# Kernel tuning notes

Hardware: AMD Instinct MI355X
Metric: run time of the kernel (lower is better)

The kernel has to match this reference:

```python
import jax, jax.numpy as jnp
from jax import lax
import numpy as np

S = 4          # tile_length
T = 16         # tile_size = S**2
K = 7          # length_inter_tile
NI = 49        # num_inter = K**2
CH_DE = 7      # design channels
EPS = 0.01
NEG = 0.01     # LeakyReLU default slope


def _conv(x, w, b, stride, pad):
    y = lax.conv_general_dilated(x, w, (stride, stride), [(pad, pad), (pad, pad)],
                                 dimension_numbers=('NCHW', 'OIHW', 'NCHW'))
    return y + b[None, :, None, None]


def _lrelu(x):
    return jax.nn.leaky_relu(x, NEG)


def _unfold(x, k=K):
    # torch F.unfold(x, k, padding=k//2): (B,C,H,W) -> (B, C*k*k, H*W), (c,i,j) ordering
    pad = k // 2
    B, C, H, W = x.shape
    xp = jnp.pad(x, ((0, 0), (0, 0), (pad, pad), (pad, pad)))
    cols = jnp.stack([xp[:, :, i:i + H, j:j + W] for i in range(k) for j in range(k)], axis=2)
    return cols.reshape(B, C * k * k, H * W)


def setup_inputs():
    key = jax.random.key(0)
    ks = jax.random.split(key, 16)
    B, H, W = 1, 48, 48
    CIN = 10; CF = 100; CW = 1024
    FINAL = T * T * NI  # 12544
    HALF = FINAL // 2   # 6272
    def w_init(k, shape, fan_in):
        return jax.random.normal(k, shape, jnp.float32) * np.float32(np.sqrt(2.0 / fan_in))
    return {
        'input': jax.random.normal(ks[0], (B, T, CIN, H, W), jnp.float32),
        'design': jax.random.normal(ks[1], (B, T, CH_DE, H, W), jnp.float32),
        'fw0': w_init(ks[2], (CF, CIN, 3, 3), CIN * 9),
        'fb0': jnp.zeros((CF,), jnp.float32),
        'fw_rest': w_init(ks[3], (13, CF, CF, 3, 3), CF * 9),
        'fb_rest': jnp.zeros((13, CF), jnp.float32),
        'ww0': w_init(ks[4], (CW, CF, S, S), CF * S * S),
        'wb0': jnp.zeros((CW,), jnp.float32),
        'ww_mid': w_init(ks[5], (3, CW, CW, 3, 3), CW * 9),
        'wb_mid': jnp.zeros((3, CW), jnp.float32),
        'ww1': w_init(ks[6], (HALF, CW, 1, 1), CW),
        'wb1': jnp.zeros((HALF,), jnp.float32),
        'ww2': w_init(ks[7], (FINAL, HALF, 1, 1), HALF),
        'wb2': jnp.zeros((FINAL,), jnp.float32),
    }


def reference(input, design, fw0, fb0, fw_rest, fb_rest, ww0, wb0, ww_mid, wb_mid, ww1, wb1, ww2, wb2):
    B, _, CIN, H, W = input.shape
    hw = H * W
    # domain: (B*hw, T, CH_DE)
    domain = design.transpose(0, 3, 4, 1, 2).reshape(B * hw, T, CH_DE)
    # X from unfolded design: (B*hw*NI, T, CH_DE)
    u = _unfold(design.reshape(B, T * CH_DE, H, W))
    X = u.reshape(B, T * CH_DE, NI, hw).transpose(0, 3, 2, 1).reshape(B * hw * NI, T, CH_DE)
    # make_full_res_img: stack tile (s*i + j) -> spatial offset (i, j)
    full = input.reshape(B, S, S, CIN, H, W).transpose(0, 3, 4, 1, 5, 2).reshape(B, CIN, H * S, W * S)
    # feature network: 14 conv3x3 + LeakyReLU at full res
    f = _lrelu(_conv(full, fw0, fb0, 1, 1))
    for i in range(fw_rest.shape[0]):
        f = _lrelu(_conv(f, fw_rest[i], fb_rest[i], 1, 1))
    g = _lrelu(_conv(f, ww0, wb0, S, 0))
    for i in range(ww_mid.shape[0]):
        g = _lrelu(_conv(g, ww_mid[i], wb_mid[i], 1, 1))
    g = _lrelu(_conv(g, ww1, wb1, 1, 0))
    Wmap = jnp.tanh(_conv(g, ww2, wb2, 1, 0))  # (B, NI*T*T, H, W)
    Wm = Wmap.reshape(B, NI, T, T, H, W).transpose(0, 4, 5, 1, 2, 3).reshape(B * hw * NI, T, T)
    Wm = Wm @ Wm.transpose(0, 2, 1) + jnp.eye(T, dtype=Wm.dtype)
    # normal equations
    XTW = X.transpose(0, 2, 1) @ Wm                                  # (N, CH_DE, T)
    A = (XTW @ X).reshape(B * hw, NI, CH_DE, CH_DE).sum(axis=1)
    A = A + EPS * jnp.eye(CH_DE, dtype=A.dtype)
    # all 3 color channels at once (same math as per-channel loop)
    Yu = _unfold(input[:, :, :3].reshape(B, T * 3, H, W))            # (B, T*3*NI, hw)
    Y = Yu.reshape(B, T, 3, NI, hw).transpose(0, 4, 3, 1, 2).reshape(B * hw * NI, T, 3)
    Bv = (XTW @ Y).reshape(B * hw, NI, CH_DE, 3).sum(axis=1)         # (B*hw, CH_DE, 3)
    para = jnp.linalg.solve(A, Bv)                                   # (B*hw, CH_DE, 3)
    out = (domain @ para).reshape(B, H, W, T, 3).transpose(0, 3, 4, 1, 2)
    return out
```

## Files before the change

kernel.cpp:

```cpp
#include <hip/hip_runtime.h>
#include <math.h>

#define LRELU(v) ((v) > 0.f ? (v) : 0.01f * (v))

typedef __attribute__((ext_vector_type(8))) short bf8v;
typedef __attribute__((ext_vector_type(4))) float f4v;

static __device__ __forceinline__ unsigned short f2b(float f) {
    unsigned int u = __float_as_uint(f);
    unsigned int r = (u + 0x7fffu + ((u >> 16) & 1u)) >> 16;
    return (unsigned short)r;
}

static __device__ __forceinline__ void gload16(const unsigned short* g, unsigned short* l) {
    __builtin_amdgcn_global_load_lds(
        (__attribute__((address_space(1))) void*)(g),
        (__attribute__((address_space(3))) void*)(l), 16, 0, 0);
}

__global__ __launch_bounds__(256) void k_build_full(const float* __restrict__ in,
                                                    unsigned short* __restrict__ full0p) {
    int idx = blockIdx.x * 256 + threadIdx.x;
    if (idx >= 368640) return;
    int c = idx % 10, pix = idx / 10;
    int X = pix % 192, Y = pix / 192;
    int t = (Y & 3) * 4 + (X & 3);
    int h = Y >> 2, w = X >> 2;
    int pp = (Y + 1) * 194 + (X + 1);
    full0p[(size_t)pp * 16 + c] = f2b(in[(((t * 10 + c) * 48) + h) * 48 + w]);
}

template <int C, int CP, int Q>
__global__ __launch_bounds__(256) void k_wcvt(const float* __restrict__ src,
                                              unsigned short* __restrict__ dst,
                                              int Mv, int Kp) {
    int m = blockIdx.x;
    for (int kp = threadIdx.x; kp < Kp; kp += 256) {
        int qq = kp / CP, c = kp - qq * CP;
        float v = 0.f;
        if (m < Mv && c < C && qq < Q)
            v = src[((size_t)m * C + c) * Q + qq];
        dst[(size_t)m * Kp + kp] = f2b(v);
    }
}

__global__ __launch_bounds__(256) void k_cvt_flat(const float* __restrict__ src,
                                                  unsigned short* __restrict__ dst,
                                                  size_t n) {
    size_t i = ((size_t)blockIdx.x * 256 + threadIdx.x) * 4;
    if (i >= n) return;
    float4 v = *(const float4*)(src + i);
    ushort4 o;
    o.x = f2b(v.x); o.y = f2b(v.y); o.z = f2b(v.z); o.w = f2b(v.w);
    *(ushort4*)(dst + i) = o;
}

__global__ __launch_bounds__(256) void k_im2col4(const unsigned short* __restrict__ src,
                                                 unsigned short* __restrict__ dst) {
    int p = blockIdx.x;
    int x = p % 48, y = p / 48;
    for (int kp = threadIdx.x; kp < 1600; kp += 256) {
        int qq = kp / 100, c = kp - qq * 100;
        int yy = y * 4 + (qq >> 2), xx = x * 4 + (qq & 3);
        dst[(size_t)p * 1600 + kp] = src[(size_t)((yy + 1) * 194 + (xx + 1)) * 104 + c];
    }
}

template <int ACT, int OF32, int REMAP, int SWZ>
__global__ __launch_bounds__(256) void k_gemm(
    const unsigned short* __restrict__ A, const unsigned short* __restrict__ Bt,
    const float* __restrict__ bias, void* __restrict__ outv,
    int K, int Mv, int ldout) {
    __shared__ __align__(16) unsigned short As[128 * 32];
    __shared__ __align__(16) unsigned short Bs[128 * 32];
    const int tid = threadIdx.x;
    const int lane = tid & 63;
    const int w = tid >> 6;
    const int wm = w >> 1, wn = w & 1;
    const int q = lane >> 4, ln = lane & 15;
    int bx = blockIdx.x, by = blockIdx.y;
    if (SWZ) {
        int gx = gridDim.x;
        int nwg = gx * gridDim.y;
        int lin = by * gx + bx;
        int qq = nwg >> 3, rr = nwg & 7;
        int xcd = lin & 7, idx = lin >> 3;
        int wg = (xcd < rr ? xcd * (qq + 1) : rr * (qq + 1) + (xcd - rr) * qq) + idx;
        bx = wg % gx; by = wg / gx;
    }
    const int m0 = by * 128, n0 = bx * 128;

    f4v acc[4][4];
#pragma unroll
    for (int i = 0; i < 4; ++i)
#pragma unroll
        for (int j = 0; j < 4; ++j) acc[i][j] = (f4v){0.f, 0.f, 0.f, 0.f};

    const int br0 = tid >> 2, bk0 = (tid & 3) << 3;
    const unsigned short* pA0 = A + (size_t)(m0 + br0) * K + bk0;
    const unsigned short* pA1 = pA0 + (size_t)64 * K;
    const unsigned short* pB0 = Bt + (size_t)(n0 + br0) * K + bk0;
    const unsigned short* pB1 = pB0 + (size_t)64 * K;
    unsigned short* lA0 = As + tid * 8;
    unsigned short* lA1 = As + 2048 + tid * 8;
    unsigned short* lB0 = Bs + tid * 8;
    unsigned short* lB1 = Bs + 2048 + tid * 8;
    const unsigned short* Ap2 = &As[(wm * 64 + ln) * 32 + q * 8];
    const unsigned short* Bp2 = &Bs[(wn * 64 + ln) * 32 + q * 8];

    for (int k0 = 0; k0 < K; k0 += 32) {
        gload16(pA0 + k0, lA0);
        gload16(pA1 + k0, lA1);
        gload16(pB0 + k0, lB0);
        gload16(pB1 + k0, lB1);
        __syncthreads();
        bf8v af[4], bfv[4];
#pragma unroll
        for (int i = 0; i < 4; ++i) af[i] = *(const bf8v*)(Ap2 + i * 512);
#pragma unroll
        for (int j = 0; j < 4; ++j) bfv[j] = *(const bf8v*)(Bp2 + j * 512);
#pragma unroll
        for (int i = 0; i < 4; ++i)
#pragma unroll
            for (int j = 0; j < 4; ++j)
                acc[i][j] = __builtin_amdgcn_mfma_f32_16x16x32_bf16(af[i], bfv[j], acc[i][j], 0, 0, 0);
        __syncthreads();
    }

    float* tb = ((float*)As) + w * 288;
#pragma unroll
    for (int i = 0; i < 4; ++i) {
        const int mbase = m0 + wm * 64 + i * 16;
        float bi[4];
#pragma unroll
        for (int r = 0; r < 4; ++r) {
            int mm = mbase + q * 4 + r;
            bi[r] = (mm < Mv) ? bias[mm] : 0.f;
        }
#pragma unroll
        for (int j = 0; j < 4; ++j) {
            const int nbase = n0 + wn * 64 + j * 16;
#pragma unroll
            for (int r = 0; r < 4; ++r) {
                float v = acc[i][j][r] + bi[r];
                v = ACT ? tanhf(v) : LRELU(v);
                tb[ln * 17 + q * 4 + r] = v;
            }
#pragma unroll
            for (int r = 0; r < 4; ++r) {
                float v = tb[(q * 4 + r) * 17 + ln];
                int n = nbase + q * 4 + r;
                int m = mbase + ln;
                if (m < Mv) {
                    if (REMAP == 3) {
                        int y = n / 48, x = n - y * 48;
                        size_t np = (size_t)((y + 1) * 50 + x + 1);
                        ((unsigned short*)outv)[np * (size_t)ldout + m] = f2b(v);
                    } else {
                        if (OF32) ((float*)outv)[(size_t)n * ldout + m] = v;
                        else ((unsigned short*)outv)[(size_t)n * ldout + m] = f2b(v);
                    }
                }
            }
        }
    }
}

template <int ACT, int OF32, int SWZ>
__global__ __launch_bounds__(512, 1) void k_gemm256(
    const unsigned short* __restrict__ A, const unsigned short* __restrict__ Bt,
    const float* __restrict__ bias, void* __restrict__ outv,
    int K, int Mv, int ldout) {
    __shared__ __align__(16) unsigned short As[2][16384];
    __shared__ __align__(16) unsigned short Bs[2][16384];
    const int tid = threadIdx.x;
    const int lane = tid & 63;
    const int w = tid >> 6;
    const int wm = w >> 2;
    const int wn = w & 3;
    const int q = lane >> 4, ln = lane & 15;

    int bx = blockIdx.x, by = blockIdx.y;
    if (SWZ) {
        int gx = gridDim.x;
        int nwg = gx * gridDim.y;
        int lin = by * gx + bx;
        int qq = nwg >> 3, rr = nwg & 7;
        int xcd = lin & 7, idx = lin >> 3;
        int wg = (xcd < rr ? xcd * (qq + 1) : rr * (qq + 1) + (xcd - rr) * qq) + idx;
        bx = wg % gx; by = wg / gx;
    }
    const int m0 = by * 256, n0 = bx * 256;

    f4v acc[8][4];
#pragma unroll
    for (int i = 0; i < 8; ++i)
#pragma unroll
        for (int j = 0; j < 4; ++j) acc[i][j] = (f4v){0.f, 0.f, 0.f, 0.f};

    const int srow = tid >> 3;
    const int sj = tid & 7;
    const int sjx = sj ^ (srow & 7);
    const unsigned short* gA = A + (size_t)(m0 + srow) * K + sjx * 8;
    const unsigned short* gB = Bt + (size_t)(n0 + srow) * K + sjx * 8;
    const size_t rstride = (size_t)64 * K;
    unsigned short* lA = &As[0][0] + tid * 8;
    unsigned short* lB = &Bs[0][0] + tid * 8;

#define STAGE256(buf, t)                                               \
    {                                                                  \
        const unsigned short* ga_ = gA + (size_t)(t) * 64;             \
        const unsigned short* gb_ = gB + (size_t)(t) * 64;             \
        unsigned short* la_ = lA + (buf) * 16384;                      \
        unsigned short* lb_ = lB + (buf) * 16384;                      \
        _Pragma("unroll")                                              \
        for (int r_ = 0; r_ < 4; ++r_) {                               \
            gload16(ga_ + r_ * rstride, la_ + r_ * 4096);              \
            gload16(gb_ + r_ * rstride, lb_ + r_ * 4096);              \
        }                                                              \
    }

    int aoff[8], boff[4];
#pragma unroll
    for (int mf = 0; mf < 8; ++mf) aoff[mf] = (wm * 128 + mf * 16 + ln) * 64;
#pragma unroll
    for (int nf = 0; nf < 4; ++nf) boff[nf] = (wn * 64 + nf * 16 + ln) * 64;
    const int l7 = ln & 7;
    const int koff0 = ((0 * 4 + q) ^ l7) * 8;
    const int koff1 = ((1 * 4 + q) ^ l7) * 8;

    const int NT = K >> 6;
    STAGE256(0, 0);
    STAGE256(1, 1);
    asm volatile("s_waitcnt vmcnt(8)" ::: "memory");
    __builtin_amdgcn_sched_barrier(0);
    __builtin_amdgcn_s_barrier();

    bf8v a0[8], b0[4], a1[8], b1[4];

    {
        const unsigned short* as = &As[0][0];
        const unsigned short* bs = &Bs[0][0];
#pragma unroll
        for (int mf = 0; mf < 8; ++mf) a0[mf] = *(const bf8v*)&as[aoff[mf] + koff0];
#pragma unroll
        for (int nf = 0; nf < 4; ++nf) b0[nf] = *(const bf8v*)&bs[boff[nf] + koff0];
#pragma unroll
        for (int mf = 0; mf < 8; ++mf) a1[mf] = *(const bf8v*)&as[aoff[mf] + koff1];
#pragma unroll
        for (int nf = 0; nf < 4; ++nf) b1[nf] = *(const bf8v*)&bs[boff[nf] + koff1];
        __builtin_amdgcn_s_setprio(1);
#pragma unroll
        for (int mf = 0; mf < 8; ++mf)
#pragma unroll
            for (int nf = 0; nf < 4; ++nf)
                acc[mf][nf] = __builtin_amdgcn_mfma_f32_16x16x32_bf16(a0[mf], b0[nf], acc[mf][nf], 0, 0, 0);
        __builtin_amdgcn_s_setprio(0);
        asm volatile("s_waitcnt lgkmcnt(0)" ::: "memory");
        __builtin_amdgcn_sched_barrier(0);
        __builtin_amdgcn_s_barrier();
        if (2 < NT) {
            STAGE256(0, 2);
            asm volatile("s_waitcnt vmcnt(8)" ::: "memory");
        } else {
            asm volatile("s_waitcnt vmcnt(0)" ::: "memory");
        }
        __builtin_amdgcn_sched_barrier(0);
        __builtin_amdgcn_s_barrier();
    }

    for (int t = 1; t < NT; ++t) {
        const int cur = t & 1;
        const unsigned short* as = &As[cur][0];
        const unsigned short* bs = &Bs[cur][0];
#pragma unroll
        for (int mf = 0; mf < 8; ++mf) a0[mf] = *(const bf8v*)&as[aoff[mf] + koff0];
#pragma unroll
        for (int nf = 0; nf < 4; ++nf) b0[nf] = *(const bf8v*)&bs[boff[nf] + koff0];
        __builtin_amdgcn_s_setprio(1);
#pragma unroll
        for (int mf = 0; mf < 8; ++mf)
#pragma unroll
            for (int nf = 0; nf < 4; ++nf)
                acc[mf][nf] = __builtin_amdgcn_mfma_f32_16x16x32_bf16(a1[mf], b1[nf], acc[mf][nf], 0, 0, 0);
        __builtin_amdgcn_s_setprio(0);
#pragma unroll
        for (int mf = 0; mf < 8; ++mf) a1[mf] = *(const bf8v*)&as[aoff[mf] + koff1];
#pragma unroll
        for (int nf = 0; nf < 4; ++nf) b1[nf] = *(const bf8v*)&bs[boff[nf] + koff1];
        __builtin_amdgcn_s_setprio(1);
#pragma unroll
        for (int mf = 0; mf < 8; ++mf)
#pragma unroll
            for (int nf = 0; nf < 4; ++nf)
                acc[mf][nf] = __builtin_amdgcn_mfma_f32_16x16x32_bf16(a0[mf], b0[nf], acc[mf][nf], 0, 0, 0);
        __builtin_amdgcn_s_setprio(0);
        asm volatile("s_waitcnt lgkmcnt(0)" ::: "memory");
        __builtin_amdgcn_sched_barrier(0);
        __builtin_amdgcn_s_barrier();
        if (t + 2 < NT) {
            STAGE256(cur, t + 2);
            asm volatile("s_waitcnt vmcnt(8)" ::: "memory");
        } else {
            asm volatile("s_waitcnt vmcnt(0)" ::: "memory");
        }
        __builtin_amdgcn_sched_barrier(0);
        __builtin_amdgcn_s_barrier();
    }
    __builtin_amdgcn_s_setprio(1);
#pragma unroll
    for (int mf = 0; mf < 8; ++mf)
#pragma unroll
        for (int nf = 0; nf < 4; ++nf)
            acc[mf][nf] = __builtin_amdgcn_mfma_f32_16x16x32_bf16(a1[mf], b1[nf], acc[mf][nf], 0, 0, 0);
    __builtin_amdgcn_s_setprio(0);
    __builtin_amdgcn_s_barrier();
#undef STAGE256

    float* tb = ((float*)&As[0][0]) + w * 288;
#pragma unroll
    for (int mf = 0; mf < 8; ++mf) {
        const int mbase = m0 + wm * 128 + mf * 16;
        float bi[4];
#pragma unroll
        for (int r = 0; r < 4; ++r) {
            int mm = mbase + q * 4 + r;
            bi[r] = (mm < Mv) ? bias[mm] : 0.f;
        }
#pragma unroll
        for (int nf = 0; nf < 4; ++nf) {
            const int nbase = n0 + wn * 64 + nf * 16;
#pragma unroll
            for (int r = 0; r < 4; ++r) {
                float v = acc[mf][nf][r] + bi[r];
                v = ACT ? tanhf(v) : LRELU(v);
                tb[ln * 17 + q * 4 + r] = v;
            }
#pragma unroll
            for (int r = 0; r < 4; ++r) {
                float v = tb[(q * 4 + r) * 17 + ln];
                int n = nbase + q * 4 + r;
                int m = mbase + ln;
                if (m < Mv) {
                    if (OF32) ((float*)outv)[(size_t)n * ldout + m] = v;
                    else ((unsigned short*)outv)[(size_t)n * ldout + m] = f2b(v);
                }
            }
        }
    }
}

template <int TAPK, int CST, int SH, int REMAP>
__global__ __launch_bounds__(256) void k_cgemm(
    const unsigned short* __restrict__ A, const unsigned short* __restrict__ Bt,
    const float* __restrict__ bias, unsigned short* __restrict__ outp,
    int Mv, int ldout) {
    __shared__ __align__(16) unsigned short As[128 * 32];
    __shared__ __align__(16) unsigned short Bs[128 * 32];
    const int tid = threadIdx.x;
    const int lane = tid & 63;
    const int w = tid >> 6;
    const int wm = w >> 1, wn = w & 1;
    const int q = lane >> 4, ln = lane & 15;
    const int m0 = blockIdx.y * 128, n0 = blockIdx.x * 128;
    const int KA = 9 * TAPK;

    f4v acc[4][4];
#pragma unroll
    for (int i = 0; i < 4; ++i)
#pragma unroll
        for (int j = 0; j < 4; ++j) acc[i][j] = (f4v){0.f, 0.f, 0.f, 0.f};

    const int br0 = tid >> 2, bk0 = (tid & 3) << 3;
    const unsigned short* pA0 = A + (size_t)(m0 + br0) * KA + bk0;
    const unsigned short* pA1 = pA0 + (size_t)64 * KA;
    unsigned short* lA0 = As + tid * 8;
    unsigned short* lA1 = As + 2048 + tid * 8;
    unsigned short* lB0 = Bs + tid * 8;
    unsigned short* lB1 = Bs + 2048 + tid * 8;
    const unsigned short* Ap2 = &As[(wm * 64 + ln) * 32 + q * 8];
    const unsigned short* Bp2 = &Bs[(wn * 64 + ln) * 32 + q * 8];

#pragma unroll
    for (int tap = 0; tap < 9; ++tap) {
        const int sh = (tap / 3 - 1) * SH + (tap % 3 - 1);
        const unsigned short* pB0 = Bt + (long)(n0 + br0 + sh) * CST + bk0;
        const unsigned short* pB1 = pB0 + (long)64 * CST;
        const int kab = tap * TAPK;
        for (int kk = 0; kk < TAPK; kk += 32) {
            gload16(pA0 + kab + kk, lA0);
            gload16(pA1 + kab + kk, lA1);
            gload16(pB0 + kk, lB0);
            gload16(pB1 + kk, lB1);
            __syncthreads();
            bf8v af[4], bfv[4];
#pragma unroll
            for (int i = 0; i < 4; ++i) af[i] = *(const bf8v*)(Ap2 + i * 512);
#pragma unroll
            for (int j = 0; j < 4; ++j) bfv[j] = *(const bf8v*)(Bp2 + j * 512);
#pragma unroll
            for (int i = 0; i < 4; ++i)
#pragma unroll
                for (int j = 0; j < 4; ++j)
                    acc[i][j] = __builtin_amdgcn_mfma_f32_16x16x32_bf16(af[i], bfv[j], acc[i][j], 0, 0, 0);
            __syncthreads();
        }
    }

    float* tb = ((float*)As) + w * 288;
#pragma unroll
    for (int i = 0; i < 4; ++i) {
        const int mbase = m0 + wm * 64 + i * 16;
        float bi[4];
#pragma unroll
        for (int r = 0; r < 4; ++r) {
            int mm = mbase + q * 4 + r;
            bi[r] = (mm < Mv) ? bias[mm] : 0.f;
        }
#pragma unroll
        for (int j = 0; j < 4; ++j) {
            const int nbase = n0 + wn * 64 + j * 16;
#pragma unroll
            for (int r = 0; r < 4; ++r) {
                float v = acc[i][j][r] + bi[r];
                v = LRELU(v);
                tb[ln * 17 + q * 4 + r] = v;
            }
#pragma unroll
            for (int r = 0; r < 4; ++r) {
                float v = tb[(q * 4 + r) * 17 + ln];
                int n = nbase + q * 4 + r;
                int m = mbase + ln;
                if (m < Mv) {
                    if (REMAP == 1) {
                        int y = n / 194, x = n - y * 194;
                        bool z = (n >= 37636) || y == 0 || y >= 193 || x == 0 || x >= 193;
                        outp[(size_t)n * ldout + m] = f2b(z ? 0.f : v);
                    } else if (REMAP == 2) {
                        int y = n / 50, x = n - y * 50;
                        bool z = (n >= 2500) || y == 0 || y >= 49 || x == 0 || x >= 49;
                        outp[(size_t)n * ldout + m] = f2b(z ? 0.f : v);
                    } else if (REMAP == 4) {
                        int y = n / 50, x = n - y * 50;
                        if (n < 2500 && y >= 1 && y <= 48 && x >= 1 && x <= 48)
                            outp[(size_t)((y - 1) * 48 + (x - 1)) * ldout + m] = f2b(v);
                    }
                }
            }
        }
    }
}

template <int TAPK, int CST, int SH, int REMAP>
__global__ __launch_bounds__(256) void k_cgemm64(
    const unsigned short* __restrict__ A, const unsigned short* __restrict__ Bt,
    const float* __restrict__ bias, unsigned short* __restrict__ outp,
    int Mv, int ldout) {
    __shared__ __align__(16) unsigned short As[64 * 32];
    __shared__ __align__(16) unsigned short Bs[128 * 32];
    const int tid = threadIdx.x;
    const int lane = tid & 63;
    const int wn = tid >> 6;
    const int q = lane >> 4, ln = lane & 15;
    const int m0 = blockIdx.y * 64, n0 = blockIdx.x * 128;
    const int KA = 9 * TAPK;

    f4v acc[4][2];
#pragma unroll
    for (int i = 0; i < 4; ++i)
#pragma unroll
        for (int j = 0; j < 2; ++j) acc[i][j] = (f4v){0.f, 0.f, 0.f, 0.f};

    const int br0 = tid >> 2, bk0 = (tid & 3) << 3;
    const unsigned short* pA0 = A + (size_t)(m0 + br0) * KA + bk0;
    unsigned short* lA0 = As + tid * 8;
    unsigned short* lB0 = Bs + tid * 8;
    unsigned short* lB1 = Bs + 2048 + tid * 8;
    const unsigned short* Ap2 = &As[ln * 32 + q * 8];
    const unsigned short* Bp2 = &Bs[(wn * 32 + ln) * 32 + q * 8];

#pragma unroll
    for (int tap = 0; tap < 9; ++tap) {
        const int sh = (tap / 3 - 1) * SH + (tap % 3 - 1);
        const unsigned short* pB0 = Bt + (long)(n0 + br0 + sh) * CST + bk0;
        const unsigned short* pB1 = pB0 + (long)64 * CST;
        const int kab = tap * TAPK;
        for (int kk = 0; kk < TAPK; kk += 32) {
            gload16(pA0 + kab + kk, lA0);
            gload16(pB0 + kk, lB0);
            gload16(pB1 + kk, lB1);
            __syncthreads();
            bf8v af[4], bfv[2];
#pragma unroll
            for (int i = 0; i < 4; ++i) af[i] = *(const bf8v*)(Ap2 + i * 512);
#pragma unroll
            for (int j = 0; j < 2; ++j) bfv[j] = *(const bf8v*)(Bp2 + j * 512);
#pragma unroll
            for (int i = 0; i < 4; ++i)
#pragma unroll
                for (int j = 0; j < 2; ++j)
                    acc[i][j] = __builtin_amdgcn_mfma_f32_16x16x32_bf16(af[i], bfv[j], acc[i][j], 0, 0, 0);
            __syncthreads();
        }
    }

    float* tb = ((float*)Bs) + wn * 288;
#pragma unroll
    for (int i = 0; i < 4; ++i) {
        const int mbase = m0 + i * 16;
        float bi[4];
#pragma unroll
        for (int r = 0; r < 4; ++r) {
            int mm = mbase + q * 4 + r;
            bi[r] = (mm < Mv) ? bias[mm] : 0.f;
        }
#pragma unroll
        for (int j = 0; j < 2; ++j) {
            const int nbase = n0 + wn * 32 + j * 16;
#pragma unroll
            for (int r = 0; r < 4; ++r) {
                float v = acc[i][j][r] + bi[r];
                v = LRELU(v);
                tb[ln * 17 + q * 4 + r] = v;
            }
#pragma unroll
            for (int r = 0; r < 4; ++r) {
                float v = tb[(q * 4 + r) * 17 + ln];
                int n = nbase + q * 4 + r;
                int m = mbase + ln;
                if (m < Mv) {
                    if (REMAP == 2) {
                        int y = n / 50, x = n - y * 50;
                        bool z = (n >= 2500) || y == 0 || y >= 49 || x == 0 || x >= 49;
                        outp[(size_t)n * ldout + m] = f2b(z ? 0.f : v);
                    } else if (REMAP == 4) {
                        int y = n / 50, x = n - y * 50;
                        if (n < 2500 && y >= 1 && y <= 48 && x >= 1 && x <= 48)
                            outp[(size_t)((y - 1) * 48 + (x - 1)) * ldout + m] = f2b(v);
                    }
                }
            }
        }
    }
}

template <int ACT, int OF32, int AF32>
__global__ __launch_bounds__(256) void k_gemm_f32a(
    const void* __restrict__ Ain, const unsigned short* __restrict__ Bt,
    const float* __restrict__ bias, void* __restrict__ outv,
    int K, int Mv, int ldout) {
    __shared__ __align__(16) unsigned short As[128 * 40];
    __shared__ __align__(16) unsigned short Bs[128 * 40];
    const int tid = threadIdx.x;
    const int lane = tid & 63;
    const int w = tid >> 6;
    const int wm = w >> 1, wn = w & 1;
    const int q = lane >> 4, ln = lane & 15;
    const int m0 = blockIdx.y * 128, n0 = blockIdx.x * 128;

    f4v acc[4][4];
#pragma unroll
    for (int i = 0; i < 4; ++i)
#pragma unroll
        for (int j = 0; j < 4; ++j) acc[i][j] = (f4v){0.f, 0.f, 0.f, 0.f};

    const int br0 = tid >> 2, bk0 = (tid & 3) << 3;
    const int br1 = br0 + 64;
    const int bl0 = br0 * 40 + bk0, bl1 = br1 * 40 + bk0;
    const unsigned short* pB0 = Bt + (size_t)(n0 + br0) * K + bk0;
    const unsigned short* pB1 = Bt + (size_t)(n0 + br1) * K + bk0;

    const unsigned short* Ab = (const unsigned short*)Ain;
    const float* Af = (const float*)Ain;
    const unsigned short* pA0 = Ab + (size_t)(m0 + br0) * K + bk0;
    const unsigned short* pA1 = Ab + (size_t)(m0 + br1) * K + bk0;
    const int fr = tid >> 3, fk = (tid & 7) << 2;
    const float* pF = Af + (size_t)(m0 + fr) * K + fk;

    for (int k0 = 0; k0 < K; k0 += 32) {
        if (AF32) {
#pragma unroll
            for (int jj = 0; jj < 4; ++jj) {
                float4 v = *(const float4*)(pF + (size_t)jj * 32 * K + k0);
                unsigned int lo = ((unsigned)f2b(v.y) << 16) | f2b(v.x);
                unsigned int hi = ((unsigned)f2b(v.w) << 16) | f2b(v.z);
                *(uint2*)&As[(fr + jj * 32) * 40 + fk] = make_uint2(lo, hi);
            }
        } else {
            uint4 a0 = *(const uint4*)(pA0 + k0);
            uint4 a1 = *(const uint4*)(pA1 + k0);
            *(uint4*)&As[bl0] = a0;
            *(uint4*)&As[bl1] = a1;
        }
        uint4 b0 = *(const uint4*)(pB0 + k0);
        uint4 b1 = *(const uint4*)(pB1 + k0);
        *(uint4*)&Bs[bl0] = b0;
        *(uint4*)&Bs[bl1] = b1;
        __syncthreads();
        const unsigned short* Ap2 = &As[(wm * 64 + ln) * 40 + q * 8];
        const unsigned short* Bp2 = &Bs[(wn * 64 + ln) * 40 + q * 8];
        bf8v af[4], bfv[4];
#pragma unroll
        for (int i = 0; i < 4; ++i) af[i] = *(const bf8v*)(Ap2 + i * 640);
#pragma unroll
        for (int j = 0; j < 4; ++j) bfv[j] = *(const bf8v*)(Bp2 + j * 640);
#pragma unroll
        for (int i = 0; i < 4; ++i)
#pragma unroll
            for (int j = 0; j < 4; ++j)
                acc[i][j] = __builtin_amdgcn_mfma_f32_16x16x32_bf16(af[i], bfv[j], acc[i][j], 0, 0, 0);
        __syncthreads();
    }

    float* tb = ((float*)As) + w * 288;
#pragma unroll
    for (int i = 0; i < 4; ++i) {
        const int mbase = m0 + wm * 64 + i * 16;
        float bi[4];
#pragma unroll
        for (int r = 0; r < 4; ++r) {
            int mm = mbase + q * 4 + r;
            bi[r] = (mm < Mv) ? bias[mm] : 0.f;
        }
#pragma unroll
        for (int j = 0; j < 4; ++j) {
            const int nbase = n0 + wn * 64 + j * 16;
#pragma unroll
            for (int r = 0; r < 4; ++r) {
                float v = acc[i][j][r] + bi[r];
                v = ACT ? tanhf(v) : LRELU(v);
                tb[ln * 17 + q * 4 + r] = v;
            }
#pragma unroll
            for (int r = 0; r < 4; ++r) {
                float v = tb[(q * 4 + r) * 17 + ln];
                size_t n = nbase + q * 4 + r;
                int m = mbase + ln;
                if (m < Mv) {
                    if (OF32) ((float*)outv)[n * (size_t)ldout + m] = v;
                    else ((unsigned short*)outv)[n * (size_t)ldout + m] = f2b(v);
                }
            }
        }
    }
}

__global__ __launch_bounds__(256) void k_solve(const float* __restrict__ WmT,
                                               const float* __restrict__ design,
                                               const float* __restrict__ input,
                                               float* __restrict__ out) {
    const int p = blockIdx.x;
    const int h = p / 48, wpx = p % 48;
    const int tid = threadIdx.x;
    __shared__ float Msh[16 * 17];
    __shared__ float Gsh[16 * 17];
    __shared__ float Xsh[16 * 8];
    __shared__ float Ysh[16 * 4];
    __shared__ float XTWsh[7 * 17];
    __shared__ float Aacc[49];
    __shared__ float Bacc[21];
    __shared__ float parash[21];

    if (tid < 49) Aacc[tid] = 0.f;
    if (tid >= 64 && tid < 85) Bacc[tid - 64] = 0.f;
    __syncthreads();

    const float* wrow = WmT + (size_t)p * 12544;
    for (int ni = 0; ni < 49; ++ni) {
        {
            int t1 = tid >> 4, t2 = tid & 15;
            Msh[t1 * 17 + t2] = wrow[ni * 256 + tid];
        }
        int sy = h + ni / 7 - 3, sx = wpx + ni % 7 - 3;
        bool inb = (sy >= 0 && sy < 48 && sx >= 0 && sx < 48);
        if (tid < 112) {
            int t = tid / 7, c = tid - t * 7;
            Xsh[t * 8 + c] = inb ? design[(size_t)(t * 7 + c) * 2304 + sy * 48 + sx] : 0.f;
        } else if (tid >= 128 && tid < 176) {
            int l = tid - 128;
            int t = l / 3, r = l - t * 3;
            Ysh[t * 4 + r] = inb ? input[(size_t)(t * 10 + r) * 2304 + sy * 48 + sx] : 0.f;
        }
        __syncthreads();
        {
            int t1 = tid >> 4, t2 = tid & 15;
            float s = (t1 == t2) ? 1.f : 0.f;
#pragma unroll
            for (int k = 0; k < 16; ++k) s += Msh[t1 * 17 + k] * Msh[t2 * 17 + k];
            Gsh[t1 * 17 + t2] = s;
        }
        __syncthreads();
        if (tid < 112) {
            int c = tid >> 4, t2 = tid & 15;
            float s = 0.f;
#pragma unroll
            for (int t1 = 0; t1 < 16; ++t1) s += Xsh[t1 * 8 + c] * Gsh[t1 * 17 + t2];
            XTWsh[c * 17 + t2] = s;
        }
        __syncthreads();
        if (tid < 49) {
            int c1 = tid / 7, c2 = tid - c1 * 7;
            float s = 0.f;
#pragma unroll
            for (int t = 0; t < 16; ++t) s += XTWsh[c1 * 17 + t] * Xsh[t * 8 + c2];
            Aacc[tid] += s;
        } else if (tid >= 64 && tid < 85) {
            int l = tid - 64;
            int c = l / 3, r = l - c * 3;
            float s = 0.f;
#pragma unroll
            for (int t = 0; t < 16; ++t) s += XTWsh[c * 17 + t] * Ysh[t * 4 + r];
            Bacc[l] += s;
        }
        __syncthreads();
    }

    if (tid == 0) {
        float Mg[7][10];
#pragma unroll
        for (int i = 0; i < 7; ++i) {
#pragma unroll
            for (int j = 0; j < 7; ++j) Mg[i][j] = Aacc[i * 7 + j] + ((i == j) ? 0.01f : 0.f);
#pragma unroll
            for (int r = 0; r < 3; ++r) Mg[i][7 + r] = Bacc[i * 3 + r];
        }
#pragma unroll
        for (int kk = 0; kk < 7; ++kk) {
            float inv = 1.f / Mg[kk][kk];
#pragma unroll
            for (int j = 0; j < 10; ++j) Mg[kk][j] *= inv;
#pragma unroll
            for (int i = 0; i < 7; ++i) {
                if (i == kk) continue;
                float f = Mg[i][kk];
#pragma unroll
                for (int j = 0; j < 10; ++j) Mg[i][j] -= f * Mg[kk][j];
            }
        }
#pragma unroll
        for (int c = 0; c < 7; ++c)
#pragma unroll
            for (int r = 0; r < 3; ++r) parash[c * 3 + r] = Mg[c][7 + r];
    }
    __syncthreads();

    if (tid < 48) {
        int t = tid / 3, r = tid - t * 3;
        float s = 0.f;
#pragma unroll
        for (int c = 0; c < 7; ++c)
            s += design[(size_t)(t * 7 + c) * 2304 + p] * parash[c * 3 + r];
        out[(size_t)tid * 2304 + p] = s;
    }
}

extern "C" void kernel_launch(void* const* d_in, const int* in_sizes, int n_in,
                              void* d_out, int out_size, void* d_ws, size_t ws_size,
                              hipStream_t stream) {
    const float* input   = (const float*)d_in[0];
    const float* design  = (const float*)d_in[1];
    const float* fw0     = (const float*)d_in[2];
    const float* fb0     = (const float*)d_in[3];
    const float* fw_rest = (const float*)d_in[4];
    const float* fb_rest = (const float*)d_in[5];
    const float* ww0     = (const float*)d_in[6];
    const float* wb0     = (const float*)d_in[7];
    const float* ww_mid  = (const float*)d_in[8];
    const float* wb_mid  = (const float*)d_in[9];
    const float* ww1     = (const float*)d_in[10];
    const float* wb1     = (const float*)d_in[11];
    const float* ww2     = (const float*)d_in[12];
    const float* wb2     = (const float*)d_in[13];
    float* out = (float*)d_out;
    float* ws = (float*)d_ws;

    float* WmT = ws;
    unsigned short* full0p = (unsigned short*)(ws + 40000);
    unsigned short* actPA  = (unsigned short*)(ws + 350000);
    unsigned short* actPB  = (unsigned short*)(ws + 2330000);
    unsigned short* fw0c   = (unsigned short*)(ws + 4310000);
    unsigned short* fwrb   = (unsigned short*)(ws + 4330000);
    unsigned short* ww0b   = (unsigned short*)(ws + 5290000);
    unsigned short* col4   = (unsigned short*)(ws + 6110000);
    unsigned short* gPA    = (unsigned short*)(ws + 7960000);
    unsigned short* gPB    = (unsigned short*)(ws + 9340000);
    unsigned short* wmb    = (unsigned short*)(ws + 10720000);
    unsigned short* gcmp   = (unsigned short*)(ws + 15440000);
    unsigned short* g1     = (unsigned short*)(ws + 28901376);
    unsigned short* ww1b   = (unsigned short*)(ws + 36126720);
    const size_t WS_BASE_F = 39337984ull;
    unsigned short* ww2b   = (unsigned short*)(ws + WS_BASE_F);
    unsigned short* ww1bp  = (unsigned short*)(ws + 59006976);
    const size_t NEED_BIG = 59006976ull + 3276800ull;

    hipMemsetAsync(full0p, 0, (size_t)37956 * 16 * 2, stream);
    hipMemsetAsync(actPA, 0, (size_t)37956 * 104 * 2, stream);
    hipMemsetAsync(actPB, 0, (size_t)37956 * 104 * 2, stream);
    hipMemsetAsync(gPA, 0, (size_t)2688 * 1024 * 2, stream);
    hipMemsetAsync(gPB, 0, (size_t)2688 * 1024 * 2, stream);

    const size_t haveF = ws_size / 4;
    const bool big = (haveF >= NEED_BIG) && (haveF >= WS_BASE_F + 39337984ull);

    k_wcvt<10, 32, 9><<<128, 256, 0, stream>>>(fw0, fw0c, 100, 288);
    for (int i = 0; i < 13; ++i)
        k_wcvt<100, 128, 9><<<128, 256, 0, stream>>>(fw_rest + (size_t)i * 90000,
                                                     fwrb + (size_t)i * 147456, 100, 1152);
    k_wcvt<100, 100, 16><<<1024, 256, 0, stream>>>(ww0, ww0b, 1024, 1600);
    if (big)
        k_wcvt<1024, 1024, 1><<<6400, 256, 0, stream>>>(ww1, ww1bp, 6272, 1024);
    else
        k_wcvt<1024, 1024, 1><<<6272, 256, 0, stream>>>(ww1, ww1b, 6272, 1024);

    k_build_full<<<1440, 256, 0, stream>>>(input, full0p);
    k_cgemm<32, 16, 194, 1><<<dim3(295, 1), 256, 0, stream>>>(fw0c, full0p, fb0, actPA, 100, 104);
    unsigned short* src = actPA;
    unsigned short* dst = actPB;
    for (int i = 0; i < 13; ++i) {
        k_cgemm<128, 104, 194, 1><<<dim3(295, 1), 256, 0, stream>>>(
            fwrb + (size_t)i * 147456, src, fb_rest + i * 100, dst, 100, 104);
        unsigned short* t = src; src = dst; dst = t;
    }

    k_im2col4<<<2304, 256, 0, stream>>>(src, col4);
    k_gemm<0, 0, 3, 0><<<dim3(18, 8), 256, 0, stream>>>(ww0b, col4, wb0, gPA, 1600, 1024, 1024);

    k_wcvt<1024, 1024, 9><<<1024, 256, 0, stream>>>(ww_mid, wmb, 1024, 9216);
    k_cgemm64<1024, 1024, 50, 2><<<dim3(20, 16), 256, 0, stream>>>(wmb, gPA, wb_mid, gPB, 1024, 1024);
    k_wcvt<1024, 1024, 9><<<1024, 256, 0, stream>>>(ww_mid + (size_t)9437184, wmb, 1024, 9216);
    k_cgemm64<1024, 1024, 50, 2><<<dim3(20, 16), 256, 0, stream>>>(wmb, gPB, wb_mid + 1024, gPA, 1024, 1024);
    k_wcvt<1024, 1024, 9><<<1024, 256, 0, stream>>>(ww_mid + (size_t)2 * 9437184, wmb, 1024, 9216);
    k_cgemm64<1024, 1024, 50, 4><<<dim3(20, 16), 256, 0, stream>>>(wmb, gPA, wb_mid + 2048, gcmp, 1024, 1024);

    if (big) {
        k_gemm256<0, 0, 1><<<dim3(9, 25), 512, 0, stream>>>(ww1bp, gcmp, wb1, g1, 1024, 6272, 6272);
        k_cvt_flat<<<76832, 256, 0, stream>>>(ww2, ww2b, (size_t)12544 * 6272);
        k_gemm256<1, 1, 1><<<dim3(9, 49), 512, 0, stream>>>(ww2b, g1, wb2, WmT, 6272, 12544, 12544);
    } else {
        k_gemm<0, 0, 0, 1><<<dim3(18, 49), 256, 0, stream>>>(ww1b, gcmp, wb1, g1, 1024, 6272, 6272);
        k_gemm_f32a<1, 1, 1><<<dim3(18, 98), 256, 0, stream>>>(ww2, g1, wb2, WmT, 6272, 12544, 12544);
    }

    k_solve<<<2304, 256, 0, stream>>>(WmT, design, input, out);
}
```

Baseline: 2.325 ms.

## Replace conv GEMMs with double-buffered 128x128 pipelined kernel and simplify gemm256 loop

Replaces the single-buffered 64x128 k_cgemm64 with k_cgemm_p, a 128x128 tile with double-buffered LDS staging via global_load_lds, XOR-swizzled layout, a 2x2 wave layout and setprio around the MFMA blocks. It is used for both the 13 feature convs and the three 1024-channel 3x3 convs. The gemm256 main loop is also restructured to load both k-halves per iteration instead of carrying a software-pipelined register prefetch across iterations. This aims to hide global-load latency and raise per-block data reuse, at the cost of more LDS (64KB) and registers per block, and it loses the register-level overlap of LDS reads with MFMAs in gemm256.

```diff
diff --git a/kernel.cpp b/kernel.cpp
--- a/kernel.cpp
+++ b/kernel.cpp
@@ -236,54 +236,15 @@
     __builtin_amdgcn_sched_barrier(0);
     __builtin_amdgcn_s_barrier();
 
-    bf8v a0[8], b0[4], a1[8], b1[4];
-
-    {
-        const unsigned short* as = &As[0][0];
-        const unsigned short* bs = &Bs[0][0];
-#pragma unroll
-        for (int mf = 0; mf < 8; ++mf) a0[mf] = *(const bf8v*)&as[aoff[mf] + koff0];
-#pragma unroll
-        for (int nf = 0; nf < 4; ++nf) b0[nf] = *(const bf8v*)&bs[boff[nf] + koff0];
-#pragma unroll
-        for (int mf = 0; mf < 8; ++mf) a1[mf] = *(const bf8v*)&as[aoff[mf] + koff1];
-#pragma unroll
-        for (int nf = 0; nf < 4; ++nf) b1[nf] = *(const bf8v*)&bs[boff[nf] + koff1];
-        __builtin_amdgcn_s_setprio(1);
-#pragma unroll
-        for (int mf = 0; mf < 8; ++mf)
-#pragma unroll
-            for (int nf = 0; nf < 4; ++nf)
-                acc[mf][nf] = __builtin_amdgcn_mfma_f32_16x16x32_bf16(a0[mf], b0[nf], acc[mf][nf], 0, 0, 0);
-        __builtin_amdgcn_s_setprio(0);
-        asm volatile("s_waitcnt lgkmcnt(0)" ::: "memory");
-        __builtin_amdgcn_sched_barrier(0);
-        __builtin_amdgcn_s_barrier();
-        if (2 < NT) {
-            STAGE256(0, 2);
-            asm volatile("s_waitcnt vmcnt(8)" ::: "memory");
-        } else {
-            asm volatile("s_waitcnt vmcnt(0)" ::: "memory");
-        }
-        __builtin_amdgcn_sched_barrier(0);
-        __builtin_amdgcn_s_barrier();
-    }
-
-    for (int t = 1; t < NT; ++t) {
+    for (int t = 0; t < NT; ++t) {
         const int cur = t & 1;
         const unsigned short* as = &As[cur][0];
         const unsigned short* bs = &Bs[cur][0];
+        bf8v a0[8], b0[4], a1[8], b1[4];
 #pragma unroll
         for (int mf = 0; mf < 8; ++mf) a0[mf] = *(const bf8v*)&as[aoff[mf] + koff0];
 #pragma unroll
         for (int nf = 0; nf < 4; ++nf) b0[nf] = *(const bf8v*)&bs[boff[nf] + koff0];
-        __builtin_amdgcn_s_setprio(1);
-#pragma unroll
-        for (int mf = 0; mf < 8; ++mf)
-#pragma unroll
-            for (int nf = 0; nf < 4; ++nf)
-                acc[mf][nf] = __builtin_amdgcn_mfma_f32_16x16x32_bf16(a1[mf], b1[nf], acc[mf][nf], 0, 0, 0);
-        __builtin_amdgcn_s_setprio(0);
 #pragma unroll
         for (int mf = 0; mf < 8; ++mf) a1[mf] = *(const bf8v*)&as[aoff[mf] + koff1];
 #pragma unroll
@@ -306,14 +267,14 @@
         }
         __builtin_amdgcn_sched_barrier(0);
         __builtin_amdgcn_s_barrier();
-    }
-    __builtin_amdgcn_s_setprio(1);
-#pragma unroll
-    for (int mf = 0; mf < 8; ++mf)
-#pragma unroll
-        for (int nf = 0; nf < 4; ++nf)
-            acc[mf][nf] = __builtin_amdgcn_mfma_f32_16x16x32_bf16(a1[mf], b1[nf], acc[mf][nf], 0, 0, 0);
-    __builtin_amdgcn_s_setprio(0);
+        __builtin_amdgcn_s_setprio(1);
+#pragma unroll
+        for (int mf = 0; mf < 8; ++mf)
+#pragma unroll
+            for (int nf = 0; nf < 4; ++nf)
+                acc[mf][nf] = __builtin_amdgcn_mfma_f32_16x16x32_bf16(a1[mf], b1[nf], acc[mf][nf], 0, 0, 0);
+        __builtin_amdgcn_s_setprio(0);
+    }
     __builtin_amdgcn_s_barrier();
 #undef STAGE256
 
@@ -452,62 +413,112 @@
 }
 
 template <int TAPK, int CST, int SH, int REMAP>
-__global__ __launch_bounds__(256) void k_cgemm64(
+__global__ __launch_bounds__(256, 1) void k_cgemm_p(
     const unsigned short* __restrict__ A, const unsigned short* __restrict__ Bt,
     const float* __restrict__ bias, unsigned short* __restrict__ outp,
     int Mv, int ldout) {
-    __shared__ __align__(16) unsigned short As[64 * 32];
-    __shared__ __align__(16) unsigned short Bs[128 * 32];
+    __shared__ __align__(16) unsigned short As[2][8192];
+    __shared__ __align__(16) unsigned short Bs[2][8192];
     const int tid = threadIdx.x;
     const int lane = tid & 63;
-    const int wn = tid >> 6;
+    const int w = tid >> 6;
+    const int wm = w >> 1, wn = w & 1;
     const int q = lane >> 4, ln = lane & 15;
-    const int m0 = blockIdx.y * 64, n0 = blockIdx.x * 128;
+    const int m0 = blockIdx.y * 128, n0 = blockIdx.x * 128;
     const int KA = 9 * TAPK;
-
-    f4v acc[4][2];
+    const int TPT = TAPK / 64;
+    const int NTT = 9 * TPT;
+
+    f4v acc[4][4];
 #pragma unroll
     for (int i = 0; i < 4; ++i)
 #pragma unroll
-        for (int j = 0; j < 2; ++j) acc[i][j] = (f4v){0.f, 0.f, 0.f, 0.f};
-
-    const int br0 = tid >> 2, bk0 = (tid & 3) << 3;
-    const unsigned short* pA0 = A + (size_t)(m0 + br0) * KA + bk0;
-    unsigned short* lA0 = As + tid * 8;
-    unsigned short* lB0 = Bs + tid * 8;
-    unsigned short* lB1 = Bs + 2048 + tid * 8;
-    const unsigned short* Ap2 = &As[ln * 32 + q * 8];
-    const unsigned short* Bp2 = &Bs[(wn * 32 + ln) * 32 + q * 8];
-
-#pragma unroll
-    for (int tap = 0; tap < 9; ++tap) {
-        const int sh = (tap / 3 - 1) * SH + (tap % 3 - 1);
-        const unsigned short* pB0 = Bt + (long)(n0 + br0 + sh) * CST + bk0;
-        const unsigned short* pB1 = pB0 + (long)64 * CST;
-        const int kab = tap * TAPK;
-        for (int kk = 0; kk < TAPK; kk += 32) {
-            gload16(pA0 + kab + kk, lA0);
-            gload16(pB0 + kk, lB0);
-            gload16(pB1 + kk, lB1);
-            __syncthreads();
-            bf8v af[4], bfv[2];
-#pragma unroll
-            for (int i = 0; i < 4; ++i) af[i] = *(const bf8v*)(Ap2 + i * 512);
-#pragma unroll
-            for (int j = 0; j < 2; ++j) bfv[j] = *(const bf8v*)(Bp2 + j * 512);
-#pragma unroll
-            for (int i = 0; i < 4; ++i)
-#pragma unroll
-                for (int j = 0; j < 2; ++j)
-                    acc[i][j] = __builtin_amdgcn_mfma_f32_16x16x32_bf16(af[i], bfv[j], acc[i][j], 0, 0, 0);
-            __syncthreads();
-        }
-    }
-
-    float* tb = ((float*)Bs) + wn * 288;
+        for (int j = 0; j < 4; ++j) acc[i][j] = (f4v){0.f, 0.f, 0.f, 0.f};
+
+    const int srow = tid >> 3;
+    const int sj = tid & 7;
+    const int sjx = sj ^ (srow & 7);
+    const unsigned short* gAx = A + (size_t)(m0 + srow) * KA + sjx * 8;
+    unsigned short* lA = &As[0][0] + tid * 8;
+    unsigned short* lB = &Bs[0][0] + tid * 8;
+
+#define STAGEP(buf, t)                                                        \
+    {                                                                         \
+        int tap_ = (t) / TPT, kk_ = ((t) - tap_ * TPT) * 64;                  \
+        int sh_ = (tap_ / 3 - 1) * SH + (tap_ % 3 - 1);                       \
+        const unsigned short* ga_ = gAx + tap_ * TAPK + kk_;                  \
+        const unsigned short* gb_ =                                           \
+            Bt + (long)(n0 + srow + sh_) * CST + kk_ + sjx * 8;               \
+        unsigned short* la_ = lA + (buf) * 8192;                              \
+        unsigned short* lb_ = lB + (buf) * 8192;                              \
+        _Pragma("unroll")                                                     \
+        for (int r_ = 0; r_ < 4; ++r_) {                                      \
+            gload16(ga_ + (size_t)r_ * 32 * KA, la_ + r_ * 2048);             \
+            gload16(gb_ + (long)r_ * 32 * CST, lb_ + r_ * 2048);              \
+        }                                                                     \
+    }
+
+    int aoff[4], boff[4];
+#pragma unroll
+    for (int mf = 0; mf < 4; ++mf) aoff[mf] = (wm * 64 + mf * 16 + ln) * 64;
+#pragma unroll
+    for (int nf = 0; nf < 4; ++nf) boff[nf] = (wn * 64 + nf * 16 + ln) * 64;
+    const int l7 = ln & 7;
+    const int koff0 = ((0 * 4 + q) ^ l7) * 8;
+    const int koff1 = ((1 * 4 + q) ^ l7) * 8;
+
+    STAGEP(0, 0);
+    STAGEP(1, 1);
+    asm volatile("s_waitcnt vmcnt(8)" ::: "memory");
+    __builtin_amdgcn_sched_barrier(0);
+    __builtin_amdgcn_s_barrier();
+
+    for (int t = 0; t < NTT; ++t) {
+        const int cur = t & 1;
+        const unsigned short* as = &As[cur][0];
+        const unsigned short* bs = &Bs[cur][0];
+        bf8v a0[4], b0[4], a1[4], b1[4];
+#pragma unroll
+        for (int mf = 0; mf < 4; ++mf) a0[mf] = *(const bf8v*)&as[aoff[mf] + koff0];
+#pragma unroll
+        for (int nf = 0; nf < 4; ++nf) b0[nf] = *(const bf8v*)&bs[boff[nf] + koff0];
+#pragma unroll
+        for (int mf = 0; mf < 4; ++mf) a1[mf] = *(const bf8v*)&as[aoff[mf] + koff1];
+#pragma unroll
+        for (int nf = 0; nf < 4; ++nf) b1[nf] = *(const bf8v*)&bs[boff[nf] + koff1];
+        __builtin_amdgcn_s_setprio(1);
+#pragma unroll
+        for (int mf = 0; mf < 4; ++mf)
+#pragma unroll
+            for (int nf = 0; nf < 4; ++nf)
+                acc[mf][nf] = __builtin_amdgcn_mfma_f32_16x16x32_bf16(a0[mf], b0[nf], acc[mf][nf], 0, 0, 0);
+        __builtin_amdgcn_s_setprio(0);
+        asm volatile("s_waitcnt lgkmcnt(0)" ::: "memory");
+        __builtin_amdgcn_sched_barrier(0);
+        __builtin_amdgcn_s_barrier();
+        if (t + 2 < NTT) {
+            STAGEP(cur, t + 2);
+            asm volatile("s_waitcnt vmcnt(8)" ::: "memory");
+        } else {
+            asm volatile("s_waitcnt vmcnt(0)" ::: "memory");
+        }
+        __builtin_amdgcn_sched_barrier(0);
+        __builtin_amdgcn_s_barrier();
+        __builtin_amdgcn_s_setprio(1);
+#pragma unroll
+        for (int mf = 0; mf < 4; ++mf)
+#pragma unroll
+            for (int nf = 0; nf < 4; ++nf)
+                acc[mf][nf] = __builtin_amdgcn_mfma_f32_16x16x32_bf16(a1[mf], b1[nf], acc[mf][nf], 0, 0, 0);
+        __builtin_amdgcn_s_setprio(0);
+    }
+    __builtin_amdgcn_s_barrier();
+#undef STAGEP
+
+    float* tb = ((float*)&As[0][0]) + w * 288;
 #pragma unroll
     for (int i = 0; i < 4; ++i) {
-        const int mbase = m0 + i * 16;
+        const int mbase = m0 + wm * 64 + i * 16;
         float bi[4];
 #pragma unroll
         for (int r = 0; r < 4; ++r) {
@@ -515,8 +526,8 @@
             bi[r] = (mm < Mv) ? bias[mm] : 0.f;
         }
 #pragma unroll
-        for (int j = 0; j < 2; ++j) {
-            const int nbase = n0 + wn * 32 + j * 16;
+        for (int j = 0; j < 4; ++j) {
+            const int nbase = n0 + wn * 64 + j * 16;
 #pragma unroll
             for (int r = 0; r < 4; ++r) {
                 float v = acc[i][j][r] + bi[r];
@@ -529,7 +540,11 @@
                 int n = nbase + q * 4 + r;
                 int m = mbase + ln;
                 if (m < Mv) {
-                    if (REMAP == 2) {
+                    if (REMAP == 1) {
+                        int y = n / 194, x = n - y * 194;
+                        bool z = (n >= 37636) || y == 0 || y >= 193 || x == 0 || x >= 193;
+                        outp[(size_t)n * ldout + m] = f2b(z ? 0.f : v);
+                    } else if (REMAP == 2) {
                         int y = n / 50, x = n - y * 50;
                         bool z = (n >= 2500) || y == 0 || y >= 49 || x == 0 || x >= 49;
                         outp[(size_t)n * ldout + m] = f2b(z ? 0.f : v);
@@ -817,7 +832,7 @@
     unsigned short* src = actPA;
     unsigned short* dst = actPB;
     for (int i = 0; i < 13; ++i) {
-        k_cgemm<128, 104, 194, 1><<<dim3(295, 1), 256, 0, stream>>>(
+        k_cgemm_p<128, 104, 194, 1><<<dim3(295, 1), 256, 0, stream>>>(
             fwrb + (size_t)i * 147456, src, fb_rest + i * 100, dst, 100, 104);
         unsigned short* t = src; src = dst; dst = t;
     }
@@ -826,11 +841,11 @@
     k_gemm<0, 0, 3, 0><<<dim3(18, 8), 256, 0, stream>>>(ww0b, col4, wb0, gPA, 1600, 1024, 1024);
 
     k_wcvt<1024, 1024, 9><<<1024, 256, 0, stream>>>(ww_mid, wmb, 1024, 9216);
-    k_cgemm64<1024, 1024, 50, 2><<<dim3(20, 16), 256, 0, stream>>>(wmb, gPA, wb_mid, gPB, 1024, 1024);
+    k_cgemm_p<1024, 1024, 50, 2><<<dim3(20, 8), 256, 0, stream>>>(wmb, gPA, wb_mid, gPB, 1024, 1024);
     k_wcvt<1024, 1024, 9><<<1024, 256, 0, stream>>>(ww_mid + (size_t)9437184, wmb, 1024, 9216);
-    k_cgemm64<1024, 1024, 50, 2><<<dim3(20, 16), 256, 0, stream>>>(wmb, gPB, wb_mid + 1024, gPA, 1024, 1024);
+    k_cgemm_p<1024, 1024, 50, 2><<<dim3(20, 8), 256, 0, stream>>>(wmb, gPB, wb_mid + 1024, gPA, 1024, 1024);
     k_wcvt<1024, 1024, 9><<<1024, 256, 0, stream>>>(ww_mid + (size_t)2 * 9437184, wmb, 1024, 9216);
-    k_cgemm64<1024, 1024, 50, 4><<<dim3(20, 16), 256, 0, stream>>>(wmb, gPA, wb_mid + 2048, gcmp, 1024, 1024);
+    k_cgemm_p<1024, 1024, 50, 4><<<dim3(20, 8), 256, 0, stream>>>(wmb, gPA, wb_mid + 2048, gcmp, 1024, 1024);
 
     if (big) {
         k_gemm256<0, 0, 1><<<dim3(9, 25), 512, 0, stream>>>(ww1bp, gcmp, wb1, g1, 1024, 6272, 6272);
```

Result: no change. 2.311 ms (-0.6%).
